# Performance work log

Hardware: AMD Instinct MI355X
Metric: run time of the kernel (lower is better)

The kernel has to match this reference:

```python
import jax, jax.numpy as jnp
import numpy as np

EMBED = 768
HIDDEN = 768
HEADS = 12
HEAD_DIM = HIDDEN // HEADS


def setup_inputs() -> dict:
    key = jax.random.key(0)
    ks = jax.random.split(key, 9)
    B, S = 16, 512
    lim = 1.0 / np.sqrt(EMBED)
    def lin(kw, kb):
        W = jax.random.uniform(kw, (EMBED, HIDDEN), jnp.float32, -lim, lim)
        b = jax.random.uniform(kb, (HIDDEN,), jnp.float32, -lim, lim)
        return W, b
    Wq, bq = lin(ks[0], ks[1])
    Wk, bk = lin(ks[2], ks[3])
    Wv, bv = lin(ks[4], ks[5])
    inp = jax.random.normal(ks[6], (B, S, EMBED), jnp.float32)
    mask = jax.random.randint(ks[7], (B, S), 0, 2).astype(jnp.float32)
    return {"input": inp, "input_mask": mask,
            "Wq": Wq, "bq": bq, "Wk": Wk, "bk": bk, "Wv": Wv, "bv": bv}


def reference(input, input_mask, Wq, bq, Wk, bk, Wv, bv):
    B, S, _ = input.shape
    # projections -> (B, H, S, D)
    def proj(W, b):
        x = jnp.einsum('bse,eh->bsh', input, W) + b
        return x.reshape(B, S, HEADS, HEAD_DIM).transpose(0, 2, 1, 3)
    Q = proj(Wq, bq)
    K = proj(Wk, bk)
    V = proj(Wv, bv)
    # scores (B, H, S, S), additive mask over keys
    scores = jnp.einsum('bhqd,bhkd->bhqk', Q, K) / jnp.sqrt(jnp.float32(HEAD_DIM))
    bias = (input_mask * -1e9)[:, None, None, :]  # (B,1,1,S) broadcast over heads & queries
    weight = jax.nn.softmax(scores + bias, axis=-1)
    out = jnp.einsum('bhqk,bhkd->bhqd', weight, V)
    return out.transpose(0, 2, 1, 3).reshape(B, S, HIDDEN)
```

## Files before the change

kernel.cpp:

```cpp
#include <hip/hip_runtime.h>
#include <hip/hip_bf16.h>
#include <cstdint>
#include <cstddef>

#define B_  16
#define S_  512
#define E_  768
#define NH_ 12
#define D_  64
#define M_  (B_*S_)

typedef unsigned short u16;
typedef __attribute__((ext_vector_type(4))) float f32x4;
typedef __attribute__((ext_vector_type(8))) short bf16x8;

#define LOG2E 1.4426950408889634f

__device__ __forceinline__ u16 f2bf(float f){
  union { float fv; uint32_t u; } v; v.fv = f;
  uint32_t u = v.u;
  uint32_t r = u + 0x7fffu + ((u >> 16) & 1u);
  return (u16)(r >> 16);
}

__device__ __forceinline__ void gload_lds16(const u16* g, u16* l){
  __builtin_amdgcn_global_load_lds(
      (const __attribute__((address_space(1))) void*)g,
      (__attribute__((address_space(3))) void*)l, 16, 0, 0);
}

__global__ __launch_bounds__(256) void prep_kernel(
    const float* __restrict__ X, u16* __restrict__ Xb,
    const float* __restrict__ Wq, const float* __restrict__ Wk,
    const float* __restrict__ Wv, u16* __restrict__ WtBase)
{
  __shared__ float t[32][33];
  const int bx = blockIdx.x;
  if (bx < 6144){
    int i = bx * 256 + threadIdx.x;
    float4 v = reinterpret_cast<const float4*>(X)[i];
    ushort4 o;
    o.x = f2bf(v.x); o.y = f2bf(v.y); o.z = f2bf(v.z); o.w = f2bf(v.w);
    reinterpret_cast<ushort4*>(Xb)[i] = o;
  } else {
    int tt = bx - 6144;
    int z = tt / 576, rem = tt % 576;
    int byi = rem / 24, bxi = rem % 24;
    const float* W = (z == 0) ? Wq : ((z == 1) ? Wk : Wv);
    u16* Wt = WtBase + (size_t)z * E_ * E_;
    int bx0 = bxi * 32, by0 = byi * 32;
    int tx = threadIdx.x & 31, ty = threadIdx.x >> 5;
    #pragma unroll
    for (int i = 0; i < 32; i += 8)
      t[ty + i][tx] = W[(size_t)(by0 + ty + i) * E_ + bx0 + tx];
    __syncthreads();
    #pragma unroll
    for (int i = 0; i < 32; i += 8)
      Wt[(size_t)(bx0 + ty + i) * E_ + by0 + tx] = f2bf(t[tx][ty + i]);
  }
}

__global__ __launch_bounds__(512) void qkv_gemm_kernel(
    const u16* __restrict__ Xb, const u16* __restrict__ WtBase,
    const float* __restrict__ bq, const float* __restrict__ bk, const float* __restrict__ bv,
    u16* __restrict__ Qb, u16* __restrict__ Kb, u16* __restrict__ VtB)
{
  extern __shared__ u16 lds[];
  u16* ldsA = lds;
  u16* ldsB = lds + 3 * 8192;

  const int z = blockIdx.z;
  const u16* Wt = WtBase + (size_t)z * E_ * E_;
  const float* bias = (z == 0) ? bq : ((z == 1) ? bk : bv);
  const int m0 = blockIdx.x * 128;
  const int n0 = blockIdx.y * 256;
  const int tid = threadIdx.x;
  const int lane = tid & 63;
  const int wave = tid >> 6;
  const int wm = wave & 1, wn = wave >> 1;
  const int col0 = lane & 15, quad = lane >> 4;
  const int rslot = quad*16 + (col0 ^ (quad << 1));
  const int oct_l = lane >> 4;
  const int row_l = (lane & 15) ^ (oct_l << 1);

  f32x4 acc[4][4];
  #pragma unroll
  for (int i = 0; i < 4; ++i)
    #pragma unroll
    for (int j = 0; j < 4; ++j)
      acc[i][j] = (f32x4){0.f, 0.f, 0.f, 0.f};

  const u16* pA  = Xb + (size_t)(m0 + wave*16 + row_l) * E_ + oct_l*8;
  const u16* pB0 = Wt + (size_t)(n0 + wave*32 + row_l) * E_ + oct_l*8;
  const u16* pB1 = pB0 + (size_t)16 * E_;

  auto stage = [&](int k0, int buf){
    u16* la = ldsA + buf * 8192;
    u16* lb = ldsB + buf * 16384;
    gload_lds16(pA  + k0,      la + (2*wave    )*512);
    gload_lds16(pA  + k0 + 32, la + (2*wave + 1)*512);
    gload_lds16(pB0 + k0,      lb + (4*wave    )*512);
    gload_lds16(pB0 + k0 + 32, lb + (4*wave + 1)*512);
    gload_lds16(pB1 + k0,      lb + (4*wave + 2)*512);
    gload_lds16(pB1 + k0 + 32, lb + (4*wave + 3)*512);
  };

  auto compute = [&](int buf){
    const u16* la = ldsA + buf * 8192;
    const u16* lb = ldsB + buf * 16384;
    #pragma unroll
    for (int ks = 0; ks < 2; ++ks){
      bf16x8 af[4], bfr[4];
      #pragma unroll
      for (int mi = 0; mi < 4; ++mi)
        af[mi] = *reinterpret_cast<const bf16x8*>(&la[((wm*4 + mi)*2 + ks)*512 + rslot*8]);
      #pragma unroll
      for (int ni = 0; ni < 4; ++ni)
        bfr[ni] = *reinterpret_cast<const bf16x8*>(&lb[((wn*4 + ni)*2 + ks)*512 + rslot*8]);
      #pragma unroll
      for (int mi = 0; mi < 4; ++mi)
        #pragma unroll
        for (int ni = 0; ni < 4; ++ni)
          acc[mi][ni] = __builtin_amdgcn_mfma_f32_16x16x32_bf16(af[mi], bfr[ni], acc[mi][ni], 0, 0, 0);
    }
  };

  stage(0, 0);
  stage(64, 1);

  #pragma unroll 1
  for (int st = 0; st < 11; ++st){
    asm volatile("s_waitcnt vmcnt(6)" ::: "memory");
    __builtin_amdgcn_s_barrier();
    __builtin_amdgcn_sched_barrier(0);
    if (st < 10) stage((st + 2) * 64, (st + 2) % 3);
    compute(st % 3);
  }
  asm volatile("s_waitcnt vmcnt(0)" ::: "memory");
  __builtin_amdgcn_s_barrier();
  __builtin_amdgcn_sched_barrier(0);
  compute(2);

  #pragma unroll
  for (int mi = 0; mi < 4; ++mi){
    #pragma unroll
    for (int ni = 0; ni < 4; ++ni){
      int n = n0 + wn*64 + ni*16 + col0;
      float bval = bias[n];
      int h = n >> 6, d = n & 63;
      #pragma unroll
      for (int r = 0; r < 4; ++r){
        int m = m0 + wm*64 + mi*16 + quad*4 + r;
        int b = m >> 9, s = m & 511;
        u16 obf = f2bf(acc[mi][ni][r] + bval);
        size_t bh = (size_t)b * NH_ + h;
        if (z == 0)      Qb[(bh * S_ + s) * D_ + d] = obf;
        else if (z == 1) Kb[(bh * S_ + s) * D_ + d] = obf;
        else             VtB[(bh * D_ + d) * S_ + s] = obf;
      }
    }
  }
}

__global__ __launch_bounds__(256) void attn_kernel(
    const u16* __restrict__ Qb, const u16* __restrict__ Kb, const u16* __restrict__ VtB,
    const float* __restrict__ mask, float* __restrict__ out)
{
  __shared__ u16 lK[2][8 * 512];
  __shared__ u16 lV[2][8 * 512];
  __shared__ u16 lP[8 * 1024];
  __shared__ float biasS[S_];
  const int bh = blockIdx.x;
  const int qt = blockIdx.y;
  const int b = bh / NH_, h = bh % NH_;
  const int tid = threadIdx.x, lane = tid & 63, wave = tid >> 6;
  const int col0 = lane & 15, quad = lane >> 4;
  const int ls = lane & 15, lk = lane >> 4;
  const float C1 = 0.125f * LOG2E;

  for (int i = tid; i < S_; i += 256)
    biasS[i] = mask[b * S_ + i] * (-1.0e9f * LOG2E);

  const u16* Kbh = Kb  + (size_t)bh * S_ * D_;
  const u16* Vbh = VtB + (size_t)bh * D_ * S_;

  bf16x8 qf[2][2];
  #pragma unroll
  for (int g = 0; g < 2; ++g){
    int qrow = qt*128 + wave*32 + g*16 + col0;
    #pragma unroll
    for (int ks = 0; ks < 2; ++ks)
      qf[g][ks] = *reinterpret_cast<const bf16x8*>(
          Qb + ((size_t)bh * S_ + qrow) * D_ + ks*32 + quad*8);
  }

  uint4 rg[4];
  auto issue = [&](int st){
    if (wave < 2){
      #pragma unroll
      for (int gg = 0; gg < 4; ++gg){
        int c = wave*4 + gg, ks = c >> 2, nt = c & 3;
        rg[gg] = *reinterpret_cast<const uint4*>(
            Kbh + (size_t)(st*64 + nt*16 + ls) * D_ + ks*32 + lk*8);
      }
    } else {
      #pragma unroll
      for (int gg = 0; gg < 4; ++gg){
        int c = (wave - 2)*4 + gg, ks2 = c >> 2, nd = c & 3;
        rg[gg] = *reinterpret_cast<const uint4*>(
            Vbh + (size_t)(nd*16 + ls) * S_ + st*64 + ks2*32 + lk*8);
      }
    }
  };
  issue(0);

  f32x4 o[2][4];
  #pragma unroll
  for (int g = 0; g < 2; ++g)
    #pragma unroll
    for (int i = 0; i < 4; ++i) o[g][i] = (f32x4){0.f, 0.f, 0.f, 0.f};
  float psum[2] = {0.f, 0.f};

  #pragma unroll 1
  for (int st = 0; st < 8; ++st){
    const int cur = st & 1;
    if (wave < 2){
      #pragma unroll
      for (int gg = 0; gg < 4; ++gg)
        *reinterpret_cast<uint4*>(&lK[cur][(wave*4 + gg)*512 + lane*8]) = rg[gg];
    } else {
      #pragma unroll
      for (int gg = 0; gg < 4; ++gg)
        *reinterpret_cast<uint4*>(&lV[cur][((wave - 2)*4 + gg)*512 + lane*8]) = rg[gg];
    }
    __syncthreads();
    if (st < 7) issue(st + 1);

    f32x4 sc[2][4];
    #pragma unroll
    for (int g = 0; g < 2; ++g)
      #pragma unroll
      for (int nt = 0; nt < 4; ++nt) sc[g][nt] = (f32x4){0.f, 0.f, 0.f, 0.f};
    #pragma unroll
    for (int ks = 0; ks < 2; ++ks){
      bf16x8 kf[4];
      #pragma unroll
      for (int nt = 0; nt < 4; ++nt)
        kf[nt] = *reinterpret_cast<const bf16x8*>(&lK[cur][(ks*4 + nt)*512 + lane*8]);
      #pragma unroll
      for (int g = 0; g < 2; ++g)
        #pragma unroll
        for (int nt = 0; nt < 4; ++nt)
          sc[g][nt] = __builtin_amdgcn_mfma_f32_16x16x32_bf16(kf[nt], qf[g][ks], sc[g][nt], 0, 0, 0);
    }

    float4 bb[4];
    #pragma unroll
    for (int nt = 0; nt < 4; ++nt)
      bb[nt] = *reinterpret_cast<const float4*>(&biasS[st*64 + nt*16 + quad*4]);

    #pragma unroll
    for (int g = 0; g < 2; ++g){
      #pragma unroll
      for (int nt = 0; nt < 4; ++nt){
        float p0 = exp2f(sc[g][nt][0] * C1 + bb[nt].x);
        float p1 = exp2f(sc[g][nt][1] * C1 + bb[nt].y);
        float p2 = exp2f(sc[g][nt][2] * C1 + bb[nt].z);
        float p3 = exp2f(sc[g][nt][3] * C1 + bb[nt].w);
        psum[g] += (p0 + p1) + (p2 + p3);
        float2 ab; ab.x = p0; ab.y = p1;
        float2 cd; cd.x = p2; cd.y = p3;
        __hip_bfloat162 h01 = __float22bfloat162_rn(ab);
        __hip_bfloat162 h23 = __float22bfloat162_rn(cd);
        uint2 pw;
        pw.x = *reinterpret_cast<unsigned int*>(&h01);
        pw.y = *reinterpret_cast<unsigned int*>(&h23);
        int addr = (wave*2 + g)*1024 + (nt >> 1)*512
                 + (((nt & 1)*2 + (quad >> 1))*16 + col0)*8 + (quad & 1)*4;
        *reinterpret_cast<uint2*>(&lP[addr]) = pw;
      }
    }

    #pragma unroll
    for (int ks2 = 0; ks2 < 2; ++ks2){
      bf16x8 pf0 = *reinterpret_cast<const bf16x8*>(&lP[(wave*2 + 0)*1024 + ks2*512 + lane*8]);
      bf16x8 pf1 = *reinterpret_cast<const bf16x8*>(&lP[(wave*2 + 1)*1024 + ks2*512 + lane*8]);
      #pragma unroll
      for (int nd = 0; nd < 4; ++nd){
        bf16x8 vf = *reinterpret_cast<const bf16x8*>(&lV[cur][(ks2*4 + nd)*512 + lane*8]);
        o[0][nd] = __builtin_amdgcn_mfma_f32_16x16x32_bf16(pf0, vf, o[0][nd], 0, 0, 0);
        o[1][nd] = __builtin_amdgcn_mfma_f32_16x16x32_bf16(pf1, vf, o[1][nd], 0, 0, 0);
      }
    }
  }

  #pragma unroll
  for (int g = 0; g < 2; ++g){
    float tot = psum[g];
    tot += __shfl_xor(tot, 16, 64);
    tot += __shfl_xor(tot, 32, 64);
    #pragma unroll
    for (int r = 0; r < 4; ++r){
      int s = qt*128 + wave*32 + g*16 + quad*4 + r;
      float lr = __shfl(tot, (lane & 48) | (quad*4 + r), 64);
      float inv = 1.0f / lr;
      #pragma unroll
      for (int nd = 0; nd < 4; ++nd){
        int d = nd*16 + col0;
        out[((size_t)b * S_ + s) * E_ + h*D_ + d] = o[g][nd][r] * inv;
      }
    }
  }
}

extern "C" void kernel_launch(void* const* d_in, const int* in_sizes, int n_in,
                              void* d_out, int out_size, void* d_ws, size_t ws_size,
                              hipStream_t stream){
  const float* X    = (const float*)d_in[0];
  const float* mask = (const float*)d_in[1];
  const float* Wq   = (const float*)d_in[2];
  const float* bq   = (const float*)d_in[3];
  const float* Wk   = (const float*)d_in[4];
  const float* bk   = (const float*)d_in[5];
  const float* Wv   = (const float*)d_in[6];
  const float* bv   = (const float*)d_in[7];
  float* out = (float*)d_out;

  u16* Xb = (u16*)d_ws;
  u16* Wt = Xb + (size_t)M_ * E_;
  u16* Qb = Wt + (size_t)3 * E_ * E_;
  u16* Kb = Qb + (size_t)M_ * E_;
  u16* Vt = Kb + (size_t)M_ * E_;

  prep_kernel<<<6144 + 1728, 256, 0, stream>>>(X, Xb, Wq, Wk, Wv, Wt);
  qkv_gemm_kernel<<<dim3(64, 3, 3), 512, 147456, stream>>>(Xb, Wt, bq, bk, bv, Qb, Kb, Vt);
  attn_kernel<<<dim3(192, 4), 256, 0, stream>>>(Qb, Kb, Vt, mask, out);
}
```

Before: 210.8 us.

## Fuse fp32-to-bf16 input conversion into QKV GEMM A-tile loading

Removes the separate X-to-bf16 conversion pass from the prep kernel. The GEMM now loads fp32 X straight into registers, packs it to bf16 and writes it to LDS itself. This saves a full write and re-read of the bf16 copy of X. The pipeline drops from triple buffering to double buffering with __syncthreads, which shrinks LDS. In exchange, each of the three z-slices re-reads fp32 X, so input traffic doubles per read, and there is less latency hiding.

```diff
diff --git a/kernel.cpp b/kernel.cpp
--- a/kernel.cpp
+++ b/kernel.cpp
@@ -29,45 +29,52 @@
       (__attribute__((address_space(3))) void*)l, 16, 0, 0);
 }
 
+__device__ __forceinline__ uint4 pack8(const float4& a, const float4& b){
+  float2 p01; p01.x = a.x; p01.y = a.y;
+  float2 p23; p23.x = a.z; p23.y = a.w;
+  float2 p45; p45.x = b.x; p45.y = b.y;
+  float2 p67; p67.x = b.z; p67.y = b.w;
+  __hip_bfloat162 h0 = __float22bfloat162_rn(p01);
+  __hip_bfloat162 h1 = __float22bfloat162_rn(p23);
+  __hip_bfloat162 h2 = __float22bfloat162_rn(p45);
+  __hip_bfloat162 h3 = __float22bfloat162_rn(p67);
+  uint4 r;
+  r.x = *reinterpret_cast<const unsigned int*>(&h0);
+  r.y = *reinterpret_cast<const unsigned int*>(&h1);
+  r.z = *reinterpret_cast<const unsigned int*>(&h2);
+  r.w = *reinterpret_cast<const unsigned int*>(&h3);
+  return r;
+}
+
 __global__ __launch_bounds__(256) void prep_kernel(
-    const float* __restrict__ X, u16* __restrict__ Xb,
     const float* __restrict__ Wq, const float* __restrict__ Wk,
     const float* __restrict__ Wv, u16* __restrict__ WtBase)
 {
   __shared__ float t[32][33];
-  const int bx = blockIdx.x;
-  if (bx < 6144){
-    int i = bx * 256 + threadIdx.x;
-    float4 v = reinterpret_cast<const float4*>(X)[i];
-    ushort4 o;
-    o.x = f2bf(v.x); o.y = f2bf(v.y); o.z = f2bf(v.z); o.w = f2bf(v.w);
-    reinterpret_cast<ushort4*>(Xb)[i] = o;
-  } else {
-    int tt = bx - 6144;
-    int z = tt / 576, rem = tt % 576;
-    int byi = rem / 24, bxi = rem % 24;
-    const float* W = (z == 0) ? Wq : ((z == 1) ? Wk : Wv);
-    u16* Wt = WtBase + (size_t)z * E_ * E_;
-    int bx0 = bxi * 32, by0 = byi * 32;
-    int tx = threadIdx.x & 31, ty = threadIdx.x >> 5;
-    #pragma unroll
-    for (int i = 0; i < 32; i += 8)
-      t[ty + i][tx] = W[(size_t)(by0 + ty + i) * E_ + bx0 + tx];
-    __syncthreads();
-    #pragma unroll
-    for (int i = 0; i < 32; i += 8)
-      Wt[(size_t)(bx0 + ty + i) * E_ + by0 + tx] = f2bf(t[tx][ty + i]);
-  }
+  const int tt = blockIdx.x;
+  int z = tt / 576, rem = tt % 576;
+  int byi = rem / 24, bxi = rem % 24;
+  const float* W = (z == 0) ? Wq : ((z == 1) ? Wk : Wv);
+  u16* Wt = WtBase + (size_t)z * E_ * E_;
+  int bx0 = bxi * 32, by0 = byi * 32;
+  int tx = threadIdx.x & 31, ty = threadIdx.x >> 5;
+  #pragma unroll
+  for (int i = 0; i < 32; i += 8)
+    t[ty + i][tx] = W[(size_t)(by0 + ty + i) * E_ + bx0 + tx];
+  __syncthreads();
+  #pragma unroll
+  for (int i = 0; i < 32; i += 8)
+    Wt[(size_t)(bx0 + ty + i) * E_ + by0 + tx] = f2bf(t[tx][ty + i]);
 }
 
 __global__ __launch_bounds__(512) void qkv_gemm_kernel(
-    const u16* __restrict__ Xb, const u16* __restrict__ WtBase,
+    const float* __restrict__ X, const u16* __restrict__ WtBase,
     const float* __restrict__ bq, const float* __restrict__ bk, const float* __restrict__ bv,
     u16* __restrict__ Qb, u16* __restrict__ Kb, u16* __restrict__ VtB)
 {
   extern __shared__ u16 lds[];
   u16* ldsA = lds;
-  u16* ldsB = lds + 3 * 8192;
+  u16* ldsB = lds + 2 * 8192;
 
   const int z = blockIdx.z;
   const u16* Wt = WtBase + (size_t)z * E_ * E_;
@@ -90,15 +97,28 @@
     for (int j = 0; j < 4; ++j)
       acc[i][j] = (f32x4){0.f, 0.f, 0.f, 0.f};
 
-  const u16* pA  = Xb + (size_t)(m0 + wave*16 + row_l) * E_ + oct_l*8;
-  const u16* pB0 = Wt + (size_t)(n0 + wave*32 + row_l) * E_ + oct_l*8;
-  const u16* pB1 = pB0 + (size_t)16 * E_;
-
-  auto stage = [&](int k0, int buf){
+  const float* pX  = X  + (size_t)(m0 + wave*16 + row_l) * E_ + oct_l*8;
+  const u16*   pB0 = Wt + (size_t)(n0 + wave*32 + row_l) * E_ + oct_l*8;
+  const u16*   pB1 = pB0 + (size_t)16 * E_;
+
+  float4 ax[4];
+  auto loadA = [&](int k0){
+    const float* p0 = pX + k0;
+    const float* p1 = pX + k0 + 32;
+    ax[0] = *reinterpret_cast<const float4*>(p0);
+    ax[1] = *reinterpret_cast<const float4*>(p0 + 4);
+    ax[2] = *reinterpret_cast<const float4*>(p1);
+    ax[3] = *reinterpret_cast<const float4*>(p1 + 4);
+  };
+  auto writeA = [&](int buf){
     u16* la = ldsA + buf * 8192;
+    uint4 w0 = pack8(ax[0], ax[1]);
+    uint4 w1 = pack8(ax[2], ax[3]);
+    *reinterpret_cast<uint4*>(&la[(2*wave    )*512 + lane*8]) = w0;
+    *reinterpret_cast<uint4*>(&la[(2*wave + 1)*512 + lane*8]) = w1;
+  };
+  auto stageB = [&](int k0, int buf){
     u16* lb = ldsB + buf * 16384;
-    gload_lds16(pA  + k0,      la + (2*wave    )*512);
-    gload_lds16(pA  + k0 + 32, la + (2*wave + 1)*512);
     gload_lds16(pB0 + k0,      lb + (4*wave    )*512);
     gload_lds16(pB0 + k0 + 32, lb + (4*wave + 1)*512);
     gload_lds16(pB1 + k0,      lb + (4*wave + 2)*512);
@@ -125,21 +145,21 @@
     }
   };
 
-  stage(0, 0);
-  stage(64, 1);
+  stageB(0, 0);
+  loadA(0);
+  writeA(0);
 
   #pragma unroll 1
-  for (int st = 0; st < 11; ++st){
-    asm volatile("s_waitcnt vmcnt(6)" ::: "memory");
-    __builtin_amdgcn_s_barrier();
-    __builtin_amdgcn_sched_barrier(0);
-    if (st < 10) stage((st + 2) * 64, (st + 2) % 3);
-    compute(st % 3);
-  }
-  asm volatile("s_waitcnt vmcnt(0)" ::: "memory");
-  __builtin_amdgcn_s_barrier();
-  __builtin_amdgcn_sched_barrier(0);
-  compute(2);
+  for (int st = 0; st < 12; ++st){
+    const int cur = st & 1;
+    __syncthreads();
+    if (st < 11){
+      stageB((st + 1) * 64, cur ^ 1);
+      loadA((st + 1) * 64);
+    }
+    compute(cur);
+    if (st < 11) writeA(cur ^ 1);
+  }
 
   #pragma unroll
   for (int mi = 0; mi < 4; ++mi){
@@ -326,13 +346,12 @@
   const float* bv   = (const float*)d_in[7];
   float* out = (float*)d_out;
 
-  u16* Xb = (u16*)d_ws;
-  u16* Wt = Xb + (size_t)M_ * E_;
+  u16* Wt = (u16*)d_ws;
   u16* Qb = Wt + (size_t)3 * E_ * E_;
   u16* Kb = Qb + (size_t)M_ * E_;
   u16* Vt = Kb + (size_t)M_ * E_;
 
-  prep_kernel<<<6144 + 1728, 256, 0, stream>>>(X, Xb, Wq, Wk, Wv, Wt);
-  qkv_gemm_kernel<<<dim3(64, 3, 3), 512, 147456, stream>>>(Xb, Wt, bq, bk, bv, Qb, Kb, Vt);
+  prep_kernel<<<1728, 256, 0, stream>>>(Wq, Wk, Wv, Wt);
+  qkv_gemm_kernel<<<dim3(64, 3, 3), 512, 98304, stream>>>(X, Wt, bq, bk, bv, Qb, Kb, Vt);
   attn_kernel<<<dim3(192, 4), 256, 0, stream>>>(Qb, Kb, Vt, mask, out);
 }
```

Measured after the change: 228.3 us. 1.08x slower.
